# Kernel tuning notes

Hardware: AMD Instinct MI355X
Metric: run time of the kernel (lower is better)

## Reference

```python
import jax, jax.numpy as jnp
import numpy as np

BETA = 1.0  # NormEMAVectorQuantizer beta

def l2norm(x, axis=-1, eps=1e-12):
    # matches torch F.normalize(p=2)
    n = jnp.sqrt(jnp.sum(x * x, axis=axis, keepdims=True))
    return x / jnp.maximum(n, eps)


def setup_inputs() -> dict:
    key = jax.random.key(0)
    k1, k2, k3, k4 = jax.random.split(key, 4)
    B, N, D, E, K = 16, 1024, 768, 32, 8192
    features = jax.random.normal(k1, (B, N, D), dtype=jnp.float32)
    # encode_task_layer: Linear(D,D) -> Tanh -> Linear(D,E), trunc_normal std=0.02, zero bias
    W1 = jax.random.normal(k2, (D, D), dtype=jnp.float32) * 0.02
    b1 = jnp.zeros((D,), dtype=jnp.float32)
    W2 = jax.random.normal(k3, (D, E), dtype=jnp.float32) * 0.02
    b2 = jnp.zeros((E,), dtype=jnp.float32)
    # EmbeddingEMA codebook is kept L2-normalized (norm_ema_inplace)
    codebook = l2norm(jax.random.normal(k4, (K, E), dtype=jnp.float32))
    return {"features": features, "W1": W1, "b1": b1, "W2": W2, "b2": b2,
            "codebook": codebook}


def reference(features, W1, b1, W2, b2, codebook):
    B, N, D = features.shape
    E = W2.shape[1]
    # encode_task_layer (fp32, as in torch autocast(enabled=False))
    h = jnp.tanh(features @ W1 + b1) @ W2 + b2          # [B, N, E]
    # NormEMAVectorQuantizer forward
    z = l2norm(h)                                       # [B, N, E]
    zf = z.reshape(-1, E)                               # [B*N, E]
    # squared-distance matrix to codebook
    d = (jnp.sum(zf * zf, axis=1, keepdims=True)
         + jnp.sum(codebook * codebook, axis=1)
         - 2.0 * zf @ codebook.T)                       # [B*N, K]
    idx = jnp.argmin(d, axis=1)                         # [B*N]
    z_q = codebook[idx].reshape(B, N, E)                # gather
    # commitment loss: beta * mse(stop_grad(z_q), z)
    loss = BETA * jnp.mean(jnp.square(jax.lax.stop_gradient(z_q) - z))
    # straight-through estimator
    z_q = z + jax.lax.stop_gradient(z_q - z)
    return z_q, loss, idx.reshape(B, N)
```

## Files before the change

### kernel.cpp

```cpp
#include <hip/hip_runtime.h>
#include <cstdint>

static constexpr int M = 16384;
static constexpr int D = 768;
static constexpr int E = 32;
static constexpr int K = 8192;

typedef _Float16 half8 __attribute__((ext_vector_type(8)));
typedef float f32x4 __attribute__((ext_vector_type(4)));

__global__ __launch_bounds__(256) void split_w1t(const float* __restrict__ W1,
    _Float16* __restrict__ W1aT, _Float16* __restrict__ W1bT)
{
  __shared__ float tile[32][33];
  const int tx = threadIdx.x & 31, ty = threadIdx.x >> 5;
  const int kb = blockIdx.x * 32, nb = blockIdx.y * 32;
#pragma unroll
  for (int i = 0; i < 4; ++i)
    tile[ty * 4 + i][tx] = W1[(size_t)(kb + ty * 4 + i) * 768 + nb + tx];
  __syncthreads();
#pragma unroll
  for (int i = 0; i < 4; ++i) {
    const int n = nb + ty * 4 + i, k = kb + tx;
    const float v = tile[tx][ty * 4 + i] * 64.0f;
    const _Float16 h = (_Float16)v;
    W1aT[(size_t)n * 768 + k] = h;
    W1bT[(size_t)n * 768 + k] = (_Float16)((v - (float)h) * 4096.0f);
  }
}

__global__ __launch_bounds__(256) void cb_prep(const float* __restrict__ CB,
    float* __restrict__ cc, _Float16* __restrict__ CBh, _Float16* __restrict__ CBr)
{
  const int k = blockIdx.x * 256 + threadIdx.x;
  const float4* p = (const float4*)(CB + (size_t)k * E);
  _Float16 hb[32], rb[32];
  float s = 0.f;
#pragma unroll
  for (int q = 0; q < 8; ++q) {
    float4 v = p[q];
    const float e[4] = {v.x, v.y, v.z, v.w};
#pragma unroll
    for (int j = 0; j < 4; ++j) {
      s += e[j] * e[j];
      const _Float16 h = (_Float16)e[j];
      hb[q * 4 + j] = h;
      rb[q * 4 + j] = (_Float16)((e[j] - (float)h) * 4096.0f);
    }
  }
  cc[k] = s;
#pragma unroll
  for (int q = 0; q < 4; ++q) {
    *(half8*)(CBh + (size_t)k * E + q * 8) = *(half8*)&hb[q * 8];
    *(half8*)(CBr + (size_t)k * E + q * 8) = *(half8*)&rb[q * 8];
  }
}

__global__ __launch_bounds__(256, 4) void gemm1_mfma(
    const float* __restrict__ X, const _Float16* __restrict__ Bag,
    const _Float16* __restrict__ Bbg, const float* __restrict__ bias,
    float* __restrict__ C)
{
  constexpr int RS = 40;
  __shared__ __align__(16) _Float16 Aa[2][64 * RS];
  __shared__ __align__(16) _Float16 Ab[2][64 * RS];
  __shared__ __align__(16) _Float16 Ba[2][64 * RS];
  __shared__ __align__(16) _Float16 Bb[2][64 * RS];

  const int t = threadIdx.x;
  const int lane = t & 63, wave = t >> 6;
  const int wm = wave >> 1, wn = wave & 1;
  const int rowBase = blockIdx.x * 64;
  const int colBase = blockIdx.y * 64;

  const int ra = t >> 2, ka = (t & 3) * 8;
  const float*    Xp  = X   + (size_t)(rowBase + ra) * D + ka;
  const _Float16* BaP = Bag + (size_t)(colBase + ra) * D + ka;
  const _Float16* BbP = Bbg + (size_t)(colBase + ra) * D + ka;
  const int woff = ra * RS + ka;

  const int arow = wm * 32 + (lane & 15);
  const int brow = wn * 32 + (lane & 15);
  const int kg = (lane >> 4) * 8;

  f32x4 accM[2][2], accR[2][2];
  const f32x4 z4 = {0.f, 0.f, 0.f, 0.f};
#pragma unroll
  for (int i = 0; i < 2; ++i)
#pragma unroll
    for (int j = 0; j < 2; ++j) { accM[i][j] = z4; accR[i][j] = z4; }

  auto cvt8 = [](float4 pa, float4 pb, half8& hi, half8& re) {
    const float v[8] = {pa.x, pa.y, pa.z, pa.w, pb.x, pb.y, pb.z, pb.w};
#pragma unroll
    for (int e = 0; e < 8; ++e) {
      const _Float16 h = (_Float16)v[e];
      hi[e] = h;
      re[e] = (_Float16)((v[e] - (float)h) * 4096.0f);
    }
  };

  {
    float4 x0 = *(const float4*)Xp;
    float4 x1 = *(const float4*)(Xp + 4);
    half8 b0 = *(const half8*)BaP;
    half8 b1 = *(const half8*)BbP;
    half8 hi, re;
    cvt8(x0, x1, hi, re);
    *(half8*)&Aa[0][woff] = hi;
    *(half8*)&Ab[0][woff] = re;
    *(half8*)&Ba[0][woff] = b0;
    *(half8*)&Bb[0][woff] = b1;
    __syncthreads();
  }

  for (int ks = 0; ks < 24; ++ks) {
    const int cur = ks & 1, nxt = cur ^ 1;
    const bool pre = (ks < 23);
    float4 nx0, nx1;
    half8 nb0, nb1;
    if (pre) {
      const int k1 = (ks + 1) * 32;
      nx0 = *(const float4*)(Xp + k1);
      nx1 = *(const float4*)(Xp + k1 + 4);
      nb0 = *(const half8*)(BaP + k1);
      nb1 = *(const half8*)(BbP + k1);
    }
    half8 aAv[2], aBv[2], bAv[2], bBv[2];
#pragma unroll
    for (int f = 0; f < 2; ++f) {
      aAv[f] = *(const half8*)&Aa[cur][(arow + f * 16) * RS + kg];
      aBv[f] = *(const half8*)&Ab[cur][(arow + f * 16) * RS + kg];
      bAv[f] = *(const half8*)&Ba[cur][(brow + f * 16) * RS + kg];
      bBv[f] = *(const half8*)&Bb[cur][(brow + f * 16) * RS + kg];
    }
#pragma unroll
    for (int fm = 0; fm < 2; ++fm)
#pragma unroll
      for (int fn = 0; fn < 2; ++fn) {
        accM[fm][fn] = __builtin_amdgcn_mfma_f32_16x16x32_f16(aAv[fm], bAv[fn], accM[fm][fn], 0, 0, 0);
        accR[fm][fn] = __builtin_amdgcn_mfma_f32_16x16x32_f16(aBv[fm], bAv[fn], accR[fm][fn], 0, 0, 0);
        accR[fm][fn] = __builtin_amdgcn_mfma_f32_16x16x32_f16(aAv[fm], bBv[fn], accR[fm][fn], 0, 0, 0);
      }
    if (pre) {
      half8 hi, re;
      cvt8(nx0, nx1, hi, re);
      *(half8*)&Aa[nxt][woff] = hi;
      *(half8*)&Ab[nxt][woff] = re;
      *(half8*)&Ba[nxt][woff] = nb0;
      *(half8*)&Bb[nxt][woff] = nb1;
    }
    __syncthreads();
  }

#pragma unroll
  for (int fm = 0; fm < 2; ++fm) {
    const int mb = rowBase + wm * 32 + fm * 16 + (lane >> 4) * 4;
#pragma unroll
    for (int fn = 0; fn < 2; ++fn) {
      const int n = colBase + wn * 32 + fn * 16 + (lane & 15);
      const float bv = bias[n];
#pragma unroll
      for (int r = 0; r < 4; ++r) {
        const float val = accM[fm][fn][r] * 0.015625f
                        + accR[fm][fn][r] * 3.814697265625e-6f + bv;
        C[(size_t)(mb + r) * D + n] = tanhf(val);
      }
    }
  }
}

__global__ __launch_bounds__(256) void gemm2_norm(
    const float* __restrict__ H, const float* __restrict__ W2,
    const float* __restrict__ b2, float* __restrict__ Z)
{
  __shared__ float Hs[32 * 132];
  __shared__ float W2s[128 * 32];
  const int t = threadIdx.x;
  const int rowBase = blockIdx.x * 32;
  const int rl = t >> 3;
  const int n0 = (t & 7) * 4;

  float acc[4] = {0.f, 0.f, 0.f, 0.f};

  for (int kc = 0; kc < D; kc += 128) {
    __syncthreads();
    for (int i = t; i < 32 * 32; i += 256) {
      const int r = i >> 5, gq = i & 31;
      *(float4*)&Hs[r * 132 + gq * 4] =
          *(const float4*)&H[(size_t)(rowBase + r) * D + kc + gq * 4];
    }
    for (int i = t; i < 1024; i += 256)
      *(float4*)&W2s[i * 4] = *(const float4*)&W2[(size_t)kc * E + i * 4];
    __syncthreads();
#pragma unroll 4
    for (int k4 = 0; k4 < 32; ++k4) {
      float4 hv = *(const float4*)&Hs[rl * 132 + k4 * 4];
      const float h[4] = {hv.x, hv.y, hv.z, hv.w};
#pragma unroll
      for (int j = 0; j < 4; ++j) {
        float4 w = *(const float4*)&W2s[(k4 * 4 + j) * E + n0];
        acc[0] = fmaf(h[j], w.x, acc[0]); acc[1] = fmaf(h[j], w.y, acc[1]);
        acc[2] = fmaf(h[j], w.z, acc[2]); acc[3] = fmaf(h[j], w.w, acc[3]);
      }
    }
  }

  float4 bb = *(const float4*)&b2[n0];
  acc[0] += bb.x; acc[1] += bb.y; acc[2] += bb.z; acc[3] += bb.w;
  float ss = acc[0] * acc[0];
  ss += acc[1] * acc[1]; ss += acc[2] * acc[2]; ss += acc[3] * acc[3];
  ss += __shfl_xor(ss, 1, 8);
  ss += __shfl_xor(ss, 2, 8);
  ss += __shfl_xor(ss, 4, 8);
  const float inv = 1.0f / fmaxf(sqrtf(ss), 1e-12f);
  float4 zv = make_float4(acc[0] * inv, acc[1] * inv, acc[2] * inv, acc[3] * inv);
  *(float4*)&Z[(size_t)(rowBase + rl) * E + n0] = zv;
}

__global__ __launch_bounds__(512) void vq_mfma(
    const float* __restrict__ Z, const float* __restrict__ CB,
    const _Float16* __restrict__ CBh, const _Float16* __restrict__ CBr,
    const float* __restrict__ ccg, float* __restrict__ zq_out,
    float* __restrict__ idx_out, float* __restrict__ lossp)
{
  __shared__ float bDs[64][4];
  __shared__ int   bIs[64][4];

  const int t = threadIdx.x;
  const int lane = t & 63, wave = t >> 6;
  const int mh = wave & 1;
  const int cq = wave >> 1;
  const int rowBase = blockIdx.x * 64;
  const int col = lane & 15, kg = lane >> 4;

  half8 zh[2], zr[2];
#pragma unroll
  for (int mt = 0; mt < 2; ++mt) {
    const float* zp = Z + (size_t)(rowBase + mh * 32 + mt * 16 + col) * E + kg * 8;
    const float4 a = *(const float4*)zp;
    const float4 b = *(const float4*)(zp + 4);
    const float v[8] = {a.x, a.y, a.z, a.w, b.x, b.y, b.z, b.w};
#pragma unroll
    for (int e = 0; e < 8; ++e) {
      const _Float16 h = (_Float16)v[e];
      zh[mt][e] = h;
      zr[mt][e] = (_Float16)((v[e] - (float)h) * 4096.0f);
    }
  }

  const f32x4 zero4 = {0.f, 0.f, 0.f, 0.f};
  float best[2][4];
  int bi[2][4];
#pragma unroll
  for (int mt = 0; mt < 2; ++mt)
#pragma unroll
    for (int r = 0; r < 4; ++r) { best[mt][r] = 3.4e38f; bi[mt][r] = 0; }

  const _Float16* ph = CBh + ((size_t)(cq * 2048 + col) * E + kg * 8);
  const _Float16* pr = CBr + ((size_t)(cq * 2048 + col) * E + kg * 8);
  const float* pc = ccg + cq * 2048 + col;
  int curIdx = cq * 2048 + col;

  for (int tt = 0; tt < 128; ++tt) {
    const half8 bh = *(const half8*)ph;
    const half8 br = *(const half8*)pr;
    const float ccv = *pc;
    ph += 16 * E; pr += 16 * E; pc += 16;
#pragma unroll
    for (int mt = 0; mt < 2; ++mt) {
      f32x4 aM = __builtin_amdgcn_mfma_f32_16x16x32_f16(zh[mt], bh, zero4, 0, 0, 0);
      f32x4 aR = __builtin_amdgcn_mfma_f32_16x16x32_f16(zr[mt], bh, zero4, 0, 0, 0);
      aR = __builtin_amdgcn_mfma_f32_16x16x32_f16(zh[mt], br, aR, 0, 0, 0);
#pragma unroll
      for (int r = 0; r < 4; ++r) {
        const float u = fmaf(aR[r], 2.44140625e-4f, aM[r]);
        const float d = fmaf(u, -2.0f, ccv);
        if (d < best[mt][r]) { best[mt][r] = d; bi[mt][r] = curIdx; }
      }
    }
    curIdx += 16;
  }

#pragma unroll
  for (int m = 1; m <= 8; m <<= 1) {
#pragma unroll
    for (int mt = 0; mt < 2; ++mt)
#pragma unroll
      for (int r = 0; r < 4; ++r) {
        const float ob = __shfl_xor(best[mt][r], m, 64);
        const int   oi = __shfl_xor(bi[mt][r],   m, 64);
        if (ob < best[mt][r] || (ob == best[mt][r] && oi < bi[mt][r])) {
          best[mt][r] = ob; bi[mt][r] = oi;
        }
      }
  }

  if (col == 0) {
#pragma unroll
    for (int mt = 0; mt < 2; ++mt)
#pragma unroll
      for (int r = 0; r < 4; ++r) {
        const int rl = mh * 32 + mt * 16 + kg * 4 + r;
        bDs[rl][cq] = best[mt][r];
        bIs[rl][cq] = bi[mt][r];
      }
  }
  __syncthreads();

  const int rl = t >> 3, part = t & 7;
  float bd = bDs[rl][0];
  int bidx = bIs[rl][0];
#pragma unroll
  for (int q = 1; q < 4; ++q)
    if (bDs[rl][q] < bd) { bd = bDs[rl][q]; bidx = bIs[rl][q]; }

  const int row = rowBase + rl;
  const float4 c4 = *(const float4*)&CB[(size_t)bidx * E + part * 4];
  const float4 z4 = *(const float4*)&Z[(size_t)row * E + part * 4];
  const float dx = c4.x - z4.x, dy = c4.y - z4.y;
  const float dz = c4.z - z4.z, dw = c4.w - z4.w;
  *(float4*)&zq_out[(size_t)row * E + part * 4] =
      make_float4(z4.x + dx, z4.y + dy, z4.z + dz, z4.w + dw);
  float ls = dx * dx;
  ls += dy * dy; ls += dz * dz; ls += dw * dw;
  ls += __shfl_xor(ls, 1, 8);
  ls += __shfl_xor(ls, 2, 8);
  ls += __shfl_xor(ls, 4, 8);
  if (part == 0) {
    lossp[row] = ls;
    idx_out[row] = (float)bidx;
  }
}

__global__ __launch_bounds__(256) void loss_reduce(const float* __restrict__ lossp, float* __restrict__ out)
{
  float s = 0.f;
  const float4* p = reinterpret_cast<const float4*>(lossp);
  for (int i = threadIdx.x; i < M / 4; i += 256) {
    float4 v = p[i];
    s += v.x + v.y + v.z + v.w;
  }
#pragma unroll
  for (int m = 32; m >= 1; m >>= 1) s += __shfl_xor(s, m, 64);
  __shared__ float red[4];
  if ((threadIdx.x & 63) == 0) red[threadIdx.x >> 6] = s;
  __syncthreads();
  if (threadIdx.x == 0)
    out[0] = (red[0] + red[1] + red[2] + red[3]) * (1.0f / (float)(M * E));
}

extern "C" void kernel_launch(void* const* d_in, const int* in_sizes, int n_in,
                              void* d_out, int out_size, void* d_ws, size_t ws_size,
                              hipStream_t stream)
{
  const float* X  = (const float*)d_in[0];
  const float* W1 = (const float*)d_in[1];
  const float* b1 = (const float*)d_in[2];
  const float* W2 = (const float*)d_in[3];
  const float* b2 = (const float*)d_in[4];
  const float* CB = (const float*)d_in[5];

  float* out  = (float*)d_out;
  float* zq   = out;
  float* loss = out + 524288;
  float* idxf = out + 524289;

  char* ws = (char*)d_ws;
  float* H1 = (float*)ws;
  float* Z  = (float*)(ws + (size_t)M * D * 4);
  float* cc = Z + (size_t)M * E;
  float* lp = cc + K;
  _Float16* W1aT = (_Float16*)(lp + M);
  _Float16* W1bT = W1aT + (size_t)D * D;
  _Float16* CBh  = W1bT + (size_t)D * D;
  _Float16* CBr  = CBh + (size_t)K * E;

  split_w1t<<<dim3(D / 32, D / 32), 256, 0, stream>>>(W1, W1aT, W1bT);
  cb_prep<<<dim3(K / 256), 256, 0, stream>>>(CB, cc, CBh, CBr);
  gemm1_mfma<<<dim3(M / 64, D / 64), 256, 0, stream>>>(X, W1aT, W1bT, b1, H1);
  gemm2_norm<<<dim3(M / 32), 256, 0, stream>>>(H1, W2, b2, Z);
  vq_mfma<<<dim3(M / 64), 512, 0, stream>>>(Z, CB, CBh, CBr, cc, zq, idxf, lp);
  loss_reduce<<<1, 256, 0, stream>>>(lp, loss);
}
```

Measured before the change: 279.8 us.

## Drop LDS staging in GEMM1 and move GEMM2 onto split-fp16 MFMA

GEMM1 no longer stages tiles through shared memory. Each wave now loads its A and B fragments straight from global memory into registers, with a larger per-wave tile (32x64) and a swapped grid order so column blocks sharing the same rows run together and can reuse them in cache. GEMM2, which was an fp32 FMA loop over LDS, becomes a split-fp16 (hi plus residual) MFMA kernel, fed by a new pre-transposed W2 and using a shuffle-based L2 norm. This removes LDS traffic and barriers, at the cost of more redundant global and L2 loads, higher register pressure, and one extra small prep launch.

```diff
diff --git a/kernel.cpp b/kernel.cpp
--- a/kernel.cpp
+++ b/kernel.cpp
@@ -29,6 +29,17 @@
   }
 }
 
+__global__ __launch_bounds__(256) void split_w2t(const float* __restrict__ W2,
+    _Float16* __restrict__ W2Th, _Float16* __restrict__ W2Tr)
+{
+  const int i = blockIdx.x * 256 + threadIdx.x;
+  const int k = i >> 5, n = i & 31;
+  const float v = W2[(size_t)k * 32 + n] * 64.0f;
+  const _Float16 h = (_Float16)v;
+  W2Th[(size_t)n * 768 + k] = h;
+  W2Tr[(size_t)n * 768 + k] = (_Float16)((v - (float)h) * 4096.0f);
+}
+
 __global__ __launch_bounds__(256) void cb_prep(const float* __restrict__ CB,
     float* __restrict__ cc, _Float16* __restrict__ CBh, _Float16* __restrict__ CBr)
 {
@@ -56,109 +67,78 @@
   }
 }
 
-__global__ __launch_bounds__(256, 4) void gemm1_mfma(
+__global__ __launch_bounds__(256, 2) void gemm1_mfma(
     const float* __restrict__ X, const _Float16* __restrict__ Bag,
     const _Float16* __restrict__ Bbg, const float* __restrict__ bias,
     float* __restrict__ C)
 {
-  constexpr int RS = 40;
-  __shared__ __align__(16) _Float16 Aa[2][64 * RS];
-  __shared__ __align__(16) _Float16 Ab[2][64 * RS];
-  __shared__ __align__(16) _Float16 Ba[2][64 * RS];
-  __shared__ __align__(16) _Float16 Bb[2][64 * RS];
-
   const int t = threadIdx.x;
   const int lane = t & 63, wave = t >> 6;
-  const int wm = wave >> 1, wn = wave & 1;
-  const int rowBase = blockIdx.x * 64;
-  const int colBase = blockIdx.y * 64;
-
-  const int ra = t >> 2, ka = (t & 3) * 8;
-  const float*    Xp  = X   + (size_t)(rowBase + ra) * D + ka;
-  const _Float16* BaP = Bag + (size_t)(colBase + ra) * D + ka;
-  const _Float16* BbP = Bbg + (size_t)(colBase + ra) * D + ka;
-  const int woff = ra * RS + ka;
-
-  const int arow = wm * 32 + (lane & 15);
-  const int brow = wn * 32 + (lane & 15);
-  const int kg = (lane >> 4) * 8;
-
-  f32x4 accM[2][2], accR[2][2];
+  const int rowBase = blockIdx.y * 128 + wave * 32;
+  const int colBase = blockIdx.x * 64;
+  const int col = lane & 15;
+  const int kg = lane >> 4;
+
+  const float* Xp0 = X + (size_t)(rowBase + col) * D + kg * 8;
+  const float* Xp1 = X + (size_t)(rowBase + 16 + col) * D + kg * 8;
+  const _Float16* BhP[4];
+  const _Float16* BrP[4];
+#pragma unroll
+  for (int fn = 0; fn < 4; ++fn) {
+    BhP[fn] = Bag + (size_t)(colBase + fn * 16 + col) * D + kg * 8;
+    BrP[fn] = Bbg + (size_t)(colBase + fn * 16 + col) * D + kg * 8;
+  }
+
+  f32x4 accM[2][4], accR[2][4];
   const f32x4 z4 = {0.f, 0.f, 0.f, 0.f};
 #pragma unroll
   for (int i = 0; i < 2; ++i)
 #pragma unroll
-    for (int j = 0; j < 2; ++j) { accM[i][j] = z4; accR[i][j] = z4; }
-
-  auto cvt8 = [](float4 pa, float4 pb, half8& hi, half8& re) {
-    const float v[8] = {pa.x, pa.y, pa.z, pa.w, pb.x, pb.y, pb.z, pb.w};
-#pragma unroll
-    for (int e = 0; e < 8; ++e) {
-      const _Float16 h = (_Float16)v[e];
-      hi[e] = h;
-      re[e] = (_Float16)((v[e] - (float)h) * 4096.0f);
-    }
-  };
-
-  {
-    float4 x0 = *(const float4*)Xp;
-    float4 x1 = *(const float4*)(Xp + 4);
-    half8 b0 = *(const half8*)BaP;
-    half8 b1 = *(const half8*)BbP;
-    half8 hi, re;
-    cvt8(x0, x1, hi, re);
-    *(half8*)&Aa[0][woff] = hi;
-    *(half8*)&Ab[0][woff] = re;
-    *(half8*)&Ba[0][woff] = b0;
-    *(half8*)&Bb[0][woff] = b1;
-    __syncthreads();
-  }
-
+    for (int j = 0; j < 4; ++j) { accM[i][j] = z4; accR[i][j] = z4; }
+
+#pragma unroll 3
   for (int ks = 0; ks < 24; ++ks) {
-    const int cur = ks & 1, nxt = cur ^ 1;
-    const bool pre = (ks < 23);
-    float4 nx0, nx1;
-    half8 nb0, nb1;
-    if (pre) {
-      const int k1 = (ks + 1) * 32;
-      nx0 = *(const float4*)(Xp + k1);
-      nx1 = *(const float4*)(Xp + k1 + 4);
-      nb0 = *(const half8*)(BaP + k1);
-      nb1 = *(const half8*)(BbP + k1);
-    }
-    half8 aAv[2], aBv[2], bAv[2], bBv[2];
-#pragma unroll
-    for (int f = 0; f < 2; ++f) {
-      aAv[f] = *(const half8*)&Aa[cur][(arow + f * 16) * RS + kg];
-      aBv[f] = *(const half8*)&Ab[cur][(arow + f * 16) * RS + kg];
-      bAv[f] = *(const half8*)&Ba[cur][(brow + f * 16) * RS + kg];
-      bBv[f] = *(const half8*)&Bb[cur][(brow + f * 16) * RS + kg];
+    const int ko = ks * 32;
+    half8 bA[4], bB[4];
+#pragma unroll
+    for (int fn = 0; fn < 4; ++fn) {
+      bA[fn] = *(const half8*)(BhP[fn] + ko);
+      bB[fn] = *(const half8*)(BrP[fn] + ko);
+    }
+    half8 aA[2], aB[2];
+    {
+      const float4 x00 = *(const float4*)(Xp0 + ko);
+      const float4 x01 = *(const float4*)(Xp0 + ko + 4);
+      const float4 x10 = *(const float4*)(Xp1 + ko);
+      const float4 x11 = *(const float4*)(Xp1 + ko + 4);
+      const float v0[8] = {x00.x, x00.y, x00.z, x00.w, x01.x, x01.y, x01.z, x01.w};
+      const float v1[8] = {x10.x, x10.y, x10.z, x10.w, x11.x, x11.y, x11.z, x11.w};
+#pragma unroll
+      for (int e = 0; e < 8; ++e) {
+        _Float16 h0 = (_Float16)v0[e];
+        aA[0][e] = h0;
+        aB[0][e] = (_Float16)((v0[e] - (float)h0) * 4096.0f);
+        _Float16 h1 = (_Float16)v1[e];
+        aA[1][e] = h1;
+        aB[1][e] = (_Float16)((v1[e] - (float)h1) * 4096.0f);
+      }
     }
 #pragma unroll
     for (int fm = 0; fm < 2; ++fm)
 #pragma unroll
-      for (int fn = 0; fn < 2; ++fn) {
-        accM[fm][fn] = __builtin_amdgcn_mfma_f32_16x16x32_f16(aAv[fm], bAv[fn], accM[fm][fn], 0, 0, 0);
-        accR[fm][fn] = __builtin_amdgcn_mfma_f32_16x16x32_f16(aBv[fm], bAv[fn], accR[fm][fn], 0, 0, 0);
-        accR[fm][fn] = __builtin_amdgcn_mfma_f32_16x16x32_f16(aAv[fm], bBv[fn], accR[fm][fn], 0, 0, 0);
-      }
-    if (pre) {
-      half8 hi, re;
-      cvt8(nx0, nx1, hi, re);
-      *(half8*)&Aa[nxt][woff] = hi;
-      *(half8*)&Ab[nxt][woff] = re;
-      *(half8*)&Ba[nxt][woff] = nb0;
-      *(half8*)&Bb[nxt][woff] = nb1;
-    }
-    __syncthreads();
+      for (int fn = 0; fn < 4; ++fn) {
+        accM[fm][fn] = __builtin_amdgcn_mfma_f32_16x16x32_f16(aA[fm], bA[fn], accM[fm][fn], 0, 0, 0);
+        accR[fm][fn] = __builtin_amdgcn_mfma_f32_16x16x32_f16(aB[fm], bA[fn], accR[fm][fn], 0, 0, 0);
+        accR[fm][fn] = __builtin_amdgcn_mfma_f32_16x16x32_f16(aA[fm], bB[fn], accR[fm][fn], 0, 0, 0);
+      }
   }
 
 #pragma unroll
   for (int fm = 0; fm < 2; ++fm) {
-    const int mb = rowBase + wm * 32 + fm * 16 + (lane >> 4) * 4;
-#pragma unroll
-    for (int fn = 0; fn < 2; ++fn) {
-      const int n = colBase + wn * 32 + fn * 16 + (lane & 15);
+    const int mb = rowBase + fm * 16 + kg * 4;
+#pragma unroll
+    for (int fn = 0; fn < 4; ++fn) {
+      const int n = colBase + fn * 16 + col;
       const float bv = bias[n];
 #pragma unroll
       for (int r = 0; r < 4; ++r) {
@@ -170,52 +150,78 @@
   }
 }
 
-__global__ __launch_bounds__(256) void gemm2_norm(
-    const float* __restrict__ H, const float* __restrict__ W2,
-    const float* __restrict__ b2, float* __restrict__ Z)
-{
-  __shared__ float Hs[32 * 132];
-  __shared__ float W2s[128 * 32];
+__global__ __launch_bounds__(256) void gemm2_mfma(
+    const float* __restrict__ H, const _Float16* __restrict__ W2Th,
+    const _Float16* __restrict__ W2Tr, const float* __restrict__ b2,
+    float* __restrict__ Z)
+{
   const int t = threadIdx.x;
-  const int rowBase = blockIdx.x * 32;
-  const int rl = t >> 3;
-  const int n0 = (t & 7) * 4;
-
-  float acc[4] = {0.f, 0.f, 0.f, 0.f};
-
-  for (int kc = 0; kc < D; kc += 128) {
-    __syncthreads();
-    for (int i = t; i < 32 * 32; i += 256) {
-      const int r = i >> 5, gq = i & 31;
-      *(float4*)&Hs[r * 132 + gq * 4] =
-          *(const float4*)&H[(size_t)(rowBase + r) * D + kc + gq * 4];
-    }
-    for (int i = t; i < 1024; i += 256)
-      *(float4*)&W2s[i * 4] = *(const float4*)&W2[(size_t)kc * E + i * 4];
-    __syncthreads();
-#pragma unroll 4
-    for (int k4 = 0; k4 < 32; ++k4) {
-      float4 hv = *(const float4*)&Hs[rl * 132 + k4 * 4];
-      const float h[4] = {hv.x, hv.y, hv.z, hv.w};
-#pragma unroll
-      for (int j = 0; j < 4; ++j) {
-        float4 w = *(const float4*)&W2s[(k4 * 4 + j) * E + n0];
-        acc[0] = fmaf(h[j], w.x, acc[0]); acc[1] = fmaf(h[j], w.y, acc[1]);
-        acc[2] = fmaf(h[j], w.z, acc[2]); acc[3] = fmaf(h[j], w.w, acc[3]);
-      }
-    }
-  }
-
-  float4 bb = *(const float4*)&b2[n0];
-  acc[0] += bb.x; acc[1] += bb.y; acc[2] += bb.z; acc[3] += bb.w;
-  float ss = acc[0] * acc[0];
-  ss += acc[1] * acc[1]; ss += acc[2] * acc[2]; ss += acc[3] * acc[3];
-  ss += __shfl_xor(ss, 1, 8);
-  ss += __shfl_xor(ss, 2, 8);
-  ss += __shfl_xor(ss, 4, 8);
-  const float inv = 1.0f / fmaxf(sqrtf(ss), 1e-12f);
-  float4 zv = make_float4(acc[0] * inv, acc[1] * inv, acc[2] * inv, acc[3] * inv);
-  *(float4*)&Z[(size_t)(rowBase + rl) * E + n0] = zv;
+  const int lane = t & 63, wave = t >> 6;
+  const int rowBase = blockIdx.x * 64 + wave * 16;
+  const int col = lane & 15;
+  const int kg = lane >> 4;
+
+  const float* Hp = H + (size_t)(rowBase + col) * D + kg * 8;
+  const _Float16* WhP[2];
+  const _Float16* WrP[2];
+#pragma unroll
+  for (int fn = 0; fn < 2; ++fn) {
+    WhP[fn] = W2Th + (size_t)(fn * 16 + col) * D + kg * 8;
+    WrP[fn] = W2Tr + (size_t)(fn * 16 + col) * D + kg * 8;
+  }
+
+  f32x4 accM[2], accR[2];
+  const f32x4 z4 = {0.f, 0.f, 0.f, 0.f};
+  accM[0] = z4; accM[1] = z4; accR[0] = z4; accR[1] = z4;
+
+#pragma unroll 3
+  for (int ks = 0; ks < 24; ++ks) {
+    const int ko = ks * 32;
+    half8 wA[2], wB[2];
+#pragma unroll
+    for (int fn = 0; fn < 2; ++fn) {
+      wA[fn] = *(const half8*)(WhP[fn] + ko);
+      wB[fn] = *(const half8*)(WrP[fn] + ko);
+    }
+    half8 hA, hB;
+    {
+      const float4 x0 = *(const float4*)(Hp + ko);
+      const float4 x1 = *(const float4*)(Hp + ko + 4);
+      const float v[8] = {x0.x, x0.y, x0.z, x0.w, x1.x, x1.y, x1.z, x1.w};
+#pragma unroll
+      for (int e = 0; e < 8; ++e) {
+        const _Float16 h = (_Float16)v[e];
+        hA[e] = h;
+        hB[e] = (_Float16)((v[e] - (float)h) * 4096.0f);
+      }
+    }
+#pragma unroll
+    for (int fn = 0; fn < 2; ++fn) {
+      accM[fn] = __builtin_amdgcn_mfma_f32_16x16x32_f16(hA, wA[fn], accM[fn], 0, 0, 0);
+      accR[fn] = __builtin_amdgcn_mfma_f32_16x16x32_f16(hB, wA[fn], accR[fn], 0, 0, 0);
+      accR[fn] = __builtin_amdgcn_mfma_f32_16x16x32_f16(hA, wB[fn], accR[fn], 0, 0, 0);
+    }
+  }
+
+  const float b0 = b2[col], b1 = b2[col + 16];
+  float v0[4], v1[4];
+#pragma unroll
+  for (int r = 0; r < 4; ++r) {
+    v0[r] = accM[0][r] * 0.015625f + accR[0][r] * 3.814697265625e-6f + b0;
+    v1[r] = accM[1][r] * 0.015625f + accR[1][r] * 3.814697265625e-6f + b1;
+  }
+#pragma unroll
+  for (int r = 0; r < 4; ++r) {
+    float ss = v0[r] * v0[r] + v1[r] * v1[r];
+    ss += __shfl_xor(ss, 1, 16);
+    ss += __shfl_xor(ss, 2, 16);
+    ss += __shfl_xor(ss, 4, 16);
+    ss += __shfl_xor(ss, 8, 16);
+    const float inv = 1.0f / fmaxf(sqrtf(ss), 1e-12f);
+    const int row = rowBase + kg * 4 + r;
+    Z[(size_t)row * E + col]      = v0[r] * inv;
+    Z[(size_t)row * E + col + 16] = v1[r] * inv;
+  }
 }
 
 __global__ __launch_bounds__(512) void vq_mfma(
@@ -375,11 +381,14 @@
   _Float16* W1bT = W1aT + (size_t)D * D;
   _Float16* CBh  = W1bT + (size_t)D * D;
   _Float16* CBr  = CBh + (size_t)K * E;
+  _Float16* W2Th = CBr + (size_t)K * E;
+  _Float16* W2Tr = W2Th + (size_t)E * D;
 
   split_w1t<<<dim3(D / 32, D / 32), 256, 0, stream>>>(W1, W1aT, W1bT);
+  split_w2t<<<dim3(D * E / 256), 256, 0, stream>>>(W2, W2Th, W2Tr);
   cb_prep<<<dim3(K / 256), 256, 0, stream>>>(CB, cc, CBh, CBr);
-  gemm1_mfma<<<dim3(M / 64, D / 64), 256, 0, stream>>>(X, W1aT, W1bT, b1, H1);
-  gemm2_norm<<<dim3(M / 32), 256, 0, stream>>>(H1, W2, b2, Z);
+  gemm1_mfma<<<dim3(D / 64, M / 128), 256, 0, stream>>>(X, W1aT, W1bT, b1, H1);
+  gemm2_mfma<<<dim3(M / 64), 256, 0, stream>>>(H1, W2Th, W2Tr, b2, Z);
   vq_mfma<<<dim3(M / 64), 512, 0, stream>>>(Z, CB, CBh, CBr, cc, zq, idxf, lp);
   loss_reduce<<<1, 256, 0, stream>>>(lp, loss);
 }
```

New measurement: 372.9 us. +33.3%, slower.
